# Kernel optimization log

Hardware: AMD Instinct MI355X
Metric: run time of the kernel (lower is better)

The kernel has to match this reference:

```python
import jax, jax.numpy as jnp
import numpy as np

N = 16384   # total nodes
E = 49152   # total edges (avg degree 3, molecular)
NG = 512    # graphs in batch
DIM = 64    # hidden dim
NF = 11     # node features
EF = 4      # edge features
HID = 128   # edge-MLP hidden
JUMPS = 3
S2S_STEPS = 3


def _gru_step(x, h, w_ih, w_hh, b_ih, b_hh):
    gi = x @ w_ih.T + b_ih
    gh = h @ w_hh.T + b_hh
    ir, iz, inn = jnp.split(gi, 3, axis=-1)
    hr, hz, hn = jnp.split(gh, 3, axis=-1)
    r = jax.nn.sigmoid(ir + hr)
    z = jax.nn.sigmoid(iz + hz)
    n = jnp.tanh(inn + r * hn)
    return (1.0 - z) * n + z * h


def _lstm_step(x, h, c, w_ih, w_hh, b_ih, b_hh):
    g = x @ w_ih.T + b_ih + h @ w_hh.T + b_hh
    i, f, gg, o = jnp.split(g, 4, axis=-1)
    c2 = jax.nn.sigmoid(f) * c + jax.nn.sigmoid(i) * jnp.tanh(gg)
    h2 = jax.nn.sigmoid(o) * jnp.tanh(c2)
    return h2, c2


def _segment_softmax(e, seg, num_segments):
    m = jax.ops.segment_max(e, seg, num_segments)
    ex = jnp.exp(e - m[seg])
    s = jax.ops.segment_sum(ex, seg, num_segments)
    return ex / s[seg]


def setup_inputs() -> dict:
    key = jax.random.key(0)
    ks = jax.random.split(key, 16)
    def rn(k, shape, s=0.05):
        return jax.random.normal(k, shape, jnp.float32) * s
    x = jax.random.normal(ks[0], (N, NF), jnp.float32)
    edge_attr = jax.random.uniform(ks[1], (E, EF), dtype=jnp.float32)
    edge_index = jax.random.randint(ks[2], (2, E), 0, N)
    batch = jnp.sort(jax.random.randint(ks[3], (N,), 0, NG))
    z = lambda n: jnp.zeros((n,), jnp.float32)
    return {
        "x": x, "edge_attr": edge_attr, "edge_index": edge_index, "batch": batch,
        "lin0_w": rn(ks[4], (DIM, NF)), "lin0_b": z(DIM),
        "mlp_w1": rn(ks[5], (HID, EF)), "mlp_b1": z(HID),
        "mlp_w2": rn(ks[6], (DIM * DIM, HID)), "mlp_b2": z(DIM * DIM),
        "conv_root": rn(ks[7], (DIM, DIM)), "conv_bias": z(DIM),
        "gru_w_ih": rn(ks[8], (3 * DIM, DIM)), "gru_w_hh": rn(ks[9], (3 * DIM, DIM)),
        "gru_b_ih": z(3 * DIM), "gru_b_hh": z(3 * DIM),
        "lstm_w_ih": rn(ks[10], (4 * DIM, 2 * DIM)), "lstm_w_hh": rn(ks[11], (4 * DIM, DIM)),
        "lstm_b_ih": z(4 * DIM), "lstm_b_hh": z(4 * DIM),
        "lin1_w": rn(ks[12], (DIM, 2 * DIM)), "lin1_b": z(DIM),
        "lin2_w": rn(ks[13], (1, DIM)), "lin2_b": z(1),
    }


def reference(x, edge_attr, edge_index, batch,
              lin0_w, lin0_b, mlp_w1, mlp_b1, mlp_w2, mlp_b2,
              conv_root, conv_bias,
              gru_w_ih, gru_w_hh, gru_b_ih, gru_b_hh,
              lstm_w_ih, lstm_w_hh, lstm_b_ih, lstm_b_hh,
              lin1_w, lin1_b, lin2_w, lin2_b):
    src, dst = edge_index[0], edge_index[1]
    out = jax.nn.relu(x @ lin0_w.T + lin0_b)           # [N, DIM]
    h = out
    # edge-conditioned weights: MLP(edge_attr) -> [E, DIM, DIM]
    ew = (jax.nn.relu(edge_attr @ mlp_w1.T + mlp_b1) @ mlp_w2.T + mlp_b2)
    ew = ew.reshape(E, DIM, DIM)
    deg = jnp.maximum(jax.ops.segment_sum(jnp.ones((E,), out.dtype), dst, N), 1.0)
    for _ in range(JUMPS):
        msg = jnp.einsum('ei,eio->eo', out[src], ew)    # gather + per-edge matvec
        agg = jax.ops.segment_sum(msg, dst, N) / deg[:, None]  # mean aggr
        m = jax.nn.relu(agg + out @ conv_root + conv_bias)
        h = _gru_step(m, h, gru_w_ih, gru_w_hh, gru_b_ih, gru_b_hh)
        out = h
    # Set2Set pooling
    qh = jnp.zeros((NG, DIM), out.dtype)
    qc = jnp.zeros((NG, DIM), out.dtype)
    q_star = jnp.zeros((NG, 2 * DIM), out.dtype)
    for _ in range(S2S_STEPS):
        qh, qc = _lstm_step(q_star, qh, qc, lstm_w_ih, lstm_w_hh, lstm_b_ih, lstm_b_hh)
        e = jnp.sum(out * qh[batch], axis=-1)           # [N]
        a = _segment_softmax(e, batch, NG)
        r = jax.ops.segment_sum(a[:, None] * out, batch, NG)  # [NG, DIM]
        q_star = jnp.concatenate([qh, r], axis=-1)
    o = jax.nn.relu(q_star @ lin1_w.T + lin1_b)
    return (o @ lin2_w.T + lin2_b).reshape(-1)
```

## Files before the change

### kernel.cpp

```cpp
#include <hip/hip_runtime.h>
#include <hip/hip_bf16.h>

#define NN 16384
#define NE 49152
#define NGR 512
#define DIM 64
#define NF 11
#define EF 4
#define HID 128
#define JUMPS 3
#define S2S 3
#define TE 192
#define SUP 49152

typedef _Float16 v8h __attribute__((ext_vector_type(8)));
typedef _Float16 v4h __attribute__((ext_vector_type(4)));
typedef float v4f __attribute__((ext_vector_type(4)));

__device__ __forceinline__ float sigmoidf_(float x) { return 1.0f / (1.0f + __expf(-x)); }

__device__ __forceinline__ void async16(const void* g, void* l) {
  __builtin_amdgcn_global_load_lds(
      (const __attribute__((address_space(1))) unsigned int*)g,
      (__attribute__((address_space(3))) unsigned int*)l, 16, 0, 0);
}

#define A0 (NN * DIM / 256)
#define A1 (A0 + NN / 256)
#define A2 (A1 + 112)
#define A3 (A2 + 192)
#define A4 (A3 + 32)
#define A5 (A4 + NN * DIM / 256)
#define A6 (A5 + 64 * 8192 / 256)
#define A7 (A6 + NE * HID / 256)
__global__ __launch_bounds__(256) void k_setup(const float* __restrict__ x,
                                               const float* __restrict__ l0w,
                                               const float* __restrict__ l0b,
                                               const float* __restrict__ ea,
                                               const float* __restrict__ w1,
                                               const float* __restrict__ b1,
                                               const float* __restrict__ w2,
                                               const float* __restrict__ conv_root,
                                               const float* __restrict__ gwih,
                                               const float* __restrict__ gwhh,
                                               const float* __restrict__ lwih,
                                               const float* __restrict__ lwhh,
                                               const float* __restrict__ l1w,
                                               float* __restrict__ out, float* __restrict__ h,
                                               _Float16* __restrict__ hid,
                                               _Float16* __restrict__ Tgo,
                                               _Float16* __restrict__ pCr,
                                               _Float16* __restrict__ pW,
                                               float* __restrict__ W2,
                                               float* __restrict__ l1T,
                                               float* __restrict__ agg, float* __restrict__ deg) {
  int b = blockIdx.x, tid = threadIdx.x;
  if (b < A0) { agg[b * 256 + tid] = 0.0f; return; }
  if (b < A1) { deg[(b - A0) * 256 + tid] = 0.0f; return; }
  if (b < A2) {
    int q = (b - A1) * 256 + tid;
    if (q < 4096) {
      int g = q >> 9, l = (q >> 3) & 63, j = q & 7;
      int ks = g >> 2, nt = g & 3;
      int k = ks * 32 + (l >> 4) * 8 + j, n = nt * 16 + (l & 15);
      pCr[q] = (_Float16)conv_root[k * 64 + n];
    } else if (q < 16384) {
      int q2 = q - 4096;
      int g = q2 >> 9, l = (q2 >> 3) & 63, j = q2 & 7;
      int ks = g / 12, nt = g % 12;
      int k = ks * 32 + (l >> 4) * 8 + j, n = nt * 16 + (l & 15);
      pW[q2] = (_Float16)gwih[n * 64 + k];
    } else {
      int q2 = q - 16384;
      int g = q2 >> 9, l = (q2 >> 3) & 63, j = q2 & 7;
      int ks = g / 12, nt = g % 12;
      int k = ks * 32 + (l >> 4) * 8 + j, n = nt * 16 + (l & 15);
      pW[12288 + q2] = (_Float16)gwhh[n * 64 + k];
    }
    return;
  }
  if (b < A3) {
    int i = (b - A2) * 256 + tid;
    int o = i / 192, k = i % 192;
    W2[i] = (k < 128) ? lwih[o * 128 + k] : lwhh[o * 64 + (k - 128)];
    return;
  }
  if (b < A4) { int i = (b - A3) * 256 + tid; int r = i / 128, c = i & 127; l1T[c * 64 + r] = l1w[i]; return; }
  if (b < A5) {
    int idx = (b - A4) * 256 + tid;
    int n = idx >> 6, d = idx & 63;
    float acc = l0b[d];
#pragma unroll
    for (int f = 0; f < NF; ++f) acc += x[n * NF + f] * l0w[d * NF + f];
    acc = fmaxf(acc, 0.0f);
    out[idx] = acc; h[idx] = acc;
    return;
  }
  if (b < A6) {
    int idx = (b - A5) * 256 + tid;
    float v = w2[idx];
    int row = idx >> 7, hh = idx & 127;
    int i = row >> 6, n = row & 63;
    int nt = n >> 4, col = n & 15;
    int ks = hh >> 5, quad = (hh >> 3) & 3, j = hh & 7;
    int t = i * 16 + ks * 4 + nt;
    Tgo[(size_t)t * 512 + (quad * 16 + col) * 8 + j] = (_Float16)v;
    return;
  }
  {
    int idx = (b - A6) * 256 + tid;
    int e = idx >> 7, hh = idx & 127;
    float acc = b1[hh];
#pragma unroll
    for (int f = 0; f < EF; ++f) acc += ea[e * EF + f] * w1[hh * EF + f];
    hid[idx] = (_Float16)fmaxf(acc, 0.0f);
  }
}

__global__ __launch_bounds__(768, 3) void k_conv(const float* __restrict__ out,
                                                 const _Float16* __restrict__ hid,
                                                 const _Float16* __restrict__ Tgo,
                                                 const int* __restrict__ src,
                                                 const int* __restrict__ dst,
                                                 float* __restrict__ agg,
                                                 float* __restrict__ deg, int count_deg) {
  __shared__ char sRing[2 * SUP];
  __shared__ _Float16 sT[64 * TE];
  __shared__ int sD[TE];
  int tid = threadIdx.x;
  int wv = tid >> 6, lane = tid & 63;
  int kh = wv & 1, nh = (wv >> 1) & 1, mh = wv >> 2;
  int col = lane & 15, quad = lane >> 4;
  int e0 = blockIdx.x * TE;
  int phase = blockIdx.x % 21;

  if (tid < TE) {
    int dn = dst[e0 + tid];
    sD[tid] = dn;
    if (count_deg) atomicAdd(&deg[dn], 1.0f);
  }
  {
    int row = tid >> 2, seg = tid & 3;
    int loc = row & 63;
    int base = (row & ~63) + (loc & 15) * 4 + (loc >> 4);
    const float* srow = out + (size_t)src[e0 + row] * DIM + seg * 16;
#pragma unroll
    for (int f = 0; f < 16; ++f)
      sT[(seg * 16 + f) * TE + base] = (_Float16)srow[f];
  }

  v8h hf[4][2];
#pragma unroll
  for (int ms = 0; ms < 4; ++ms) {
    const _Float16* hrow = hid + (size_t)(e0 + mh * 64 + ms * 16 + col) * HID + kh * 64 + quad * 8;
#pragma unroll
    for (int k2 = 0; k2 < 2; ++k2) hf[ms][k2] = *(const v8h*)(hrow + k2 * 32);
  }

  __syncthreads();
  asm volatile("s_waitcnt vmcnt(0)" ::: "memory");

  const char* TgoB = (const char*)Tgo;
#pragma unroll
  for (int p = 0; p < 2; ++p) {
    int op = phase + p; if (op >= 21) op -= 21;
    const char* gp = TgoB + (size_t)op * SUP + wv * 4096 + lane * 16;
    char* lp = sRing + p * SUP + wv * 4096;
#pragma unroll
    for (int j = 0; j < 4; ++j) async16(gp + j * 1024, lp + j * 1024);
  }

  v4f acc[4][2];
#pragma unroll
  for (int ms = 0; ms < 4; ++ms)
#pragma unroll
    for (int nt = 0; nt < 2; ++nt) acc[ms][nt] = (v4f)(0.0f);

  for (int t = 0; t < 21; ++t) {
    int ot = phase + t; if (ot >= 21) ot -= 21;
    if (t < 20) asm volatile("s_waitcnt vmcnt(4)" ::: "memory");
    else        asm volatile("s_waitcnt vmcnt(0)" ::: "memory");
    asm volatile("s_barrier" ::: "memory");
    const char* sbase = sRing + (t & 1) * SUP;
#pragma unroll
    for (int cc = 0; cc < 3; ++cc) {
      int sp = ot * 3 + cc;
      const char* rb = sbase + cc * 16384;
      v8h bfr[2][2];
#pragma unroll
      for (int k2 = 0; k2 < 2; ++k2)
#pragma unroll
        for (int nt = 0; nt < 2; ++nt)
          bfr[k2][nt] = *(const v8h*)(rb + (((kh * 2 + k2) * 4 + nh * 2 + nt) * 64 + lane) * 16);
      v4h s4 = *(const v4h*)&sT[sp * TE + mh * 64 + col * 4];
#pragma unroll
      for (int ms = 0; ms < 4; ++ms) {
        _Float16 sv = s4[ms];
        v8h s8 = {sv, sv, sv, sv, sv, sv, sv, sv};
#pragma unroll
        for (int k2 = 0; k2 < 2; ++k2) {
          v8h az = hf[ms][k2] * s8;
#pragma unroll
          for (int nt = 0; nt < 2; ++nt)
            acc[ms][nt] = __builtin_amdgcn_mfma_f32_16x16x32_f16(az, bfr[k2][nt], acc[ms][nt], 0, 0, 0);
        }
      }
    }
    asm volatile("s_waitcnt lgkmcnt(0)" ::: "memory");
    if (t + 2 < 21) {
      int o2 = phase + t + 2; if (o2 >= 21) o2 -= 21;
      const char* gp = TgoB + (size_t)o2 * SUP + wv * 4096 + lane * 16;
      char* lp = sRing + (t & 1) * SUP + wv * 4096;
#pragma unroll
      for (int j = 0; j < 4; ++j) async16(gp + j * 1024, lp + j * 1024);
    }
  }

  if (wv < 4) {
    const char* gp = TgoB + (size_t)63 * 16384 + wv * 4096 + lane * 16;
    char* lp = sRing + SUP + wv * 4096;
#pragma unroll
    for (int j = 0; j < 4; ++j) async16(gp + j * 1024, lp + j * 1024);
  }
  asm volatile("s_waitcnt vmcnt(0)" ::: "memory");
  asm volatile("s_barrier" ::: "memory");
  {
    const char* rb = sRing + SUP;
    v8h bfr[2][2];
#pragma unroll
    for (int k2 = 0; k2 < 2; ++k2)
#pragma unroll
      for (int nt = 0; nt < 2; ++nt)
        bfr[k2][nt] = *(const v8h*)(rb + (((kh * 2 + k2) * 4 + nh * 2 + nt) * 64 + lane) * 16);
    v4h s4 = *(const v4h*)&sT[63 * TE + mh * 64 + col * 4];
#pragma unroll
    for (int ms = 0; ms < 4; ++ms) {
      _Float16 sv = s4[ms];
      v8h s8 = {sv, sv, sv, sv, sv, sv, sv, sv};
#pragma unroll
      for (int k2 = 0; k2 < 2; ++k2) {
        v8h az = hf[ms][k2] * s8;
#pragma unroll
        for (int nt = 0; nt < 2; ++nt)
          acc[ms][nt] = __builtin_amdgcn_mfma_f32_16x16x32_f16(az, bfr[k2][nt], acc[ms][nt], 0, 0, 0);
      }
    }
  }

  __syncthreads();
  float* aggL = (float*)sRing;
  if (kh == 0) {
#pragma unroll
    for (int ms = 0; ms < 4; ++ms)
#pragma unroll
      for (int r = 0; r < 4; ++r) {
        int row = mh * 64 + ms * 16 + quad * 4 + r;
#pragma unroll
        for (int nt = 0; nt < 2; ++nt)
          aggL[row * 65 + (nh * 2 + nt) * 16 + col] = acc[ms][nt][r];
      }
  }
  __syncthreads();
  if (kh == 1) {
#pragma unroll
    for (int ms = 0; ms < 4; ++ms)
#pragma unroll
      for (int r = 0; r < 4; ++r) {
        int row = mh * 64 + ms * 16 + quad * 4 + r;
#pragma unroll
        for (int nt = 0; nt < 2; ++nt) {
          int a = row * 65 + (nh * 2 + nt) * 16 + col;
          aggL[a] += acc[ms][nt][r];
        }
      }
  }
  __syncthreads();
  for (int idx = tid; idx < TE * 64; idx += 768) {
    int row = idx >> 6, c = idx & 63;
    atomicAdd(agg + (size_t)sD[row] * DIM + c, aggL[row * 65 + c]);
  }
}

__global__ __launch_bounds__(256) void k_gru(float* __restrict__ agg,
                                             const float* __restrict__ deg,
                                             const _Float16* __restrict__ pCr,
                                             const _Float16* __restrict__ pW,
                                             const float* __restrict__ conv_bias,
                                             const float* __restrict__ bih,
                                             const float* __restrict__ bhh,
                                             float* __restrict__ out, float* __restrict__ h) {
  __shared__ _Float16 sW[24576];
  __shared__ _Float16 sMf[64][72];
  int tid = threadIdx.x;
  int w = tid >> 6, lane = tid & 63, col = lane & 15, quad = lane >> 4;
  int n0 = blockIdx.x * 64;
  int mrow = n0 + w * 16 + col;

  {
    int off = w * 12288 + lane * 16;
#pragma unroll
    for (int j = 0; j < 12; ++j)
      async16((const char*)pW + off + j * 1024, (char*)sW + off + j * 1024);
  }

  v8h afO[2], afH[2];
#pragma unroll
  for (int ks = 0; ks < 2; ++ks) {
    const float* p = out + (size_t)mrow * DIM + ks * 32 + quad * 8;
    float4 a = *(const float4*)p, b = *(const float4*)(p + 4);
    afO[ks] = (v8h){(_Float16)a.x, (_Float16)a.y, (_Float16)a.z, (_Float16)a.w,
                    (_Float16)b.x, (_Float16)b.y, (_Float16)b.z, (_Float16)b.w};
    const float* q = h + (size_t)mrow * DIM + ks * 32 + quad * 8;
    float4 c = *(const float4*)q, d = *(const float4*)(q + 4);
    afH[ks] = (v8h){(_Float16)c.x, (_Float16)c.y, (_Float16)c.z, (_Float16)c.w,
                    (_Float16)d.x, (_Float16)d.y, (_Float16)d.z, (_Float16)d.w};
  }

  v4f accC[4];
#pragma unroll
  for (int nt = 0; nt < 4; ++nt) accC[nt] = (v4f)(0.0f);
#pragma unroll
  for (int ks = 0; ks < 2; ++ks)
#pragma unroll
    for (int nt = 0; nt < 4; ++nt) {
      v8h bf = *(const v8h*)(pCr + (ks * 4 + nt) * 512 + lane * 8);
      accC[nt] = __builtin_amdgcn_mfma_f32_16x16x32_f16(afO[ks], bf, accC[nt], 0, 0, 0);
    }

#pragma unroll
  for (int r = 0; r < 4; ++r) {
    int nd = n0 + w * 16 + quad * 4 + r;
    float dg = fmaxf(deg[nd], 1.0f);
#pragma unroll
    for (int nt = 0; nt < 4; ++nt) {
      int o = nt * 16 + col;
      float mv = fmaxf(agg[(size_t)nd * DIM + o] / dg + accC[nt][r] + conv_bias[o], 0.0f);
      agg[(size_t)nd * DIM + o] = 0.0f;
      sMf[nd - n0][o] = (_Float16)mv;
    }
  }
  __syncthreads();

  v8h afM[2];
#pragma unroll
  for (int ks = 0; ks < 2; ++ks)
    afM[ks] = *(const v8h*)&sMf[w * 16 + col][ks * 32 + quad * 8];

  v4f aRZ[8], aIN[4], aHN[4];
#pragma unroll
  for (int t = 0; t < 8; ++t) aRZ[t] = (v4f)(0.0f);
#pragma unroll
  for (int t = 0; t < 4; ++t) { aIN[t] = (v4f)(0.0f); aHN[t] = (v4f)(0.0f); }
#pragma unroll
  for (int ks = 0; ks < 2; ++ks) {
#pragma unroll
    for (int nt = 0; nt < 8; ++nt) {
      v8h bf1 = *(const v8h*)(sW + (ks * 12 + nt) * 512 + lane * 8);
      aRZ[nt] = __builtin_amdgcn_mfma_f32_16x16x32_f16(afM[ks], bf1, aRZ[nt], 0, 0, 0);
      v8h bf2 = *(const v8h*)(sW + 12288 + (ks * 12 + nt) * 512 + lane * 8);
      aRZ[nt] = __builtin_amdgcn_mfma_f32_16x16x32_f16(afH[ks], bf2, aRZ[nt], 0, 0, 0);
    }
#pragma unroll
    for (int nt = 8; nt < 12; ++nt) {
      v8h bf1 = *(const v8h*)(sW + (ks * 12 + nt) * 512 + lane * 8);
      aIN[nt - 8] = __builtin_amdgcn_mfma_f32_16x16x32_f16(afM[ks], bf1, aIN[nt - 8], 0, 0, 0);
      v8h bf2 = *(const v8h*)(sW + 12288 + (ks * 12 + nt) * 512 + lane * 8);
      aHN[nt - 8] = __builtin_amdgcn_mfma_f32_16x16x32_f16(afH[ks], bf2, aHN[nt - 8], 0, 0, 0);
    }
  }

#pragma unroll
  for (int r = 0; r < 4; ++r) {
    int nd = n0 + w * 16 + quad * 4 + r;
#pragma unroll
    for (int nt = 0; nt < 4; ++nt) {
      int d = nt * 16 + col;
      float rv = sigmoidf_(aRZ[nt][r] + bih[d] + bhh[d]);
      float zv = sigmoidf_(aRZ[nt + 4][r] + bih[64 + d] + bhh[64 + d]);
      float nv = tanhf(aIN[nt][r] + bih[128 + d] + rv * (aHN[nt][r] + bhh[128 + d]));
      float hold = h[(size_t)nd * DIM + d];
      float hn = (1.0f - zv) * nv + zv * hold;
      h[(size_t)nd * DIM + d] = hn;
      out[(size_t)nd * DIM + d] = hn;
    }
  }
}

__global__ __launch_bounds__(256) void k_s2s(const float* __restrict__ out,
                                             const int* __restrict__ batch,
                                             const float* __restrict__ W2,
                                             const float* __restrict__ lbih,
                                             const float* __restrict__ lbhh,
                                             const float* __restrict__ l1T,
                                             const float* __restrict__ l1b,
                                             const float* __restrict__ l2w,
                                             const float* __restrict__ l2b,
                                             float* __restrict__ outp) {
  __shared__ float sOut[128][64];
  __shared__ __align__(16) float sQ[192];
  __shared__ float sQc[64], sG[256], sR[4][64], sEv[256];
  __shared__ float sMv, sSum;
  __shared__ int sRange[2];
  int g = blockIdx.x, tid = threadIdx.x;
  int wv = tid >> 6, ln = tid & 63;

  if (tid < 2) {
    int target = g + tid;
    int lo = 0, hi = NN;
    while (lo < hi) { int mid = (lo + hi) >> 1; if (batch[mid] < target) lo = mid + 1; else hi = mid; }
    sRange[tid] = lo;
  }
  if (tid < 192) sQ[tid] = 0.0f;
  if (tid < 64) sQc[tid] = 0.0f;
  __syncthreads();
  int s0 = sRange[0], cnt = sRange[1] - sRange[0];
  int stg = cnt < 128 ? cnt : 128;
  for (int r = wv; r < stg; r += 4) sOut[r][ln] = out[(size_t)(s0 + r) * DIM + ln];
  __syncthreads();

  const float* wrow = W2 + (size_t)tid * 192;
  float bias = lbih[tid] + lbhh[tid];

  for (int step = 0; step < S2S; ++step) {
    v4f a4[8];
#pragma unroll
    for (int s = 0; s < 8; ++s) a4[s] = (v4f)(0.0f);
#pragma unroll
    for (int kb = 0; kb < 48; ++kb) {
      v4f w4 = *(const v4f*)(wrow + kb * 4);
      v4f q4 = *(const v4f*)&sQ[kb * 4];
      a4[kb & 7] += w4 * q4;
    }
    v4f t4 = a4[0] + a4[1] + a4[2] + a4[3] + a4[4] + a4[5] + a4[6] + a4[7];
    sG[tid] = bias + t4[0] + t4[1] + t4[2] + t4[3];
    __syncthreads();
    if (tid < 64) {
      float gi = sG[tid], gf = sG[64 + tid], gg = sG[128 + tid], go = sG[192 + tid];
      float c2 = sigmoidf_(gf) * sQc[tid] + sigmoidf_(gi) * tanhf(gg);
      sQc[tid] = c2;
      sQ[128 + tid] = sigmoidf_(go) * tanhf(c2);
    }
    __syncthreads();
    for (int r = wv; r < cnt; r += 4) {
      float v = (r < 128) ? sOut[r][ln] : out[(size_t)(s0 + r) * DIM + ln];
      float p = v * sQ[128 + ln];
#pragma unroll
      for (int off = 32; off >= 1; off >>= 1) p += __shfl_xor(p, off);
      if (ln == 0 && r < 256) sEv[r] = p;
    }
    __syncthreads();
    if (wv == 0) {
      float mv = -1e30f;
      for (int r = ln; r < cnt; r += 64) mv = fmaxf(mv, sEv[r]);
#pragma unroll
      for (int off = 32; off >= 1; off >>= 1) mv = fmaxf(mv, __shfl_xor(mv, off));
      float ss = 0.0f;
      for (int r = ln; r < cnt; r += 64) ss += __expf(sEv[r] - mv);
#pragma unroll
      for (int off = 32; off >= 1; off >>= 1) ss += __shfl_xor(ss, off);
      if (ln == 0) { sMv = mv; sSum = ss; }
    }
    __syncthreads();
    float racc = 0.0f;
    for (int r = wv; r < cnt; r += 4) {
      float w = __expf(sEv[r] - sMv);
      float v = (r < 128) ? sOut[r][ln] : out[(size_t)(s0 + r) * DIM + ln];
      racc += w * v;
    }
    sR[wv][ln] = racc;
    __syncthreads();
    if (tid < 64) {
      float rv = sR[0][tid] + sR[1][tid] + sR[2][tid] + sR[3][tid];
      rv = (cnt > 0 && sSum > 0.0f) ? rv / sSum : 0.0f;
      sQ[tid] = sQ[128 + tid];
      sQ[64 + tid] = rv;
    }
    __syncthreads();
  }
  if (wv == 0) {
    float acc = l1b[ln];
#pragma unroll 4
    for (int k = 0; k < 128; ++k) acc += sQ[k] * l1T[k * 64 + ln];
    acc = fmaxf(acc, 0.0f);
    float p = acc * l2w[ln];
#pragma unroll
    for (int off = 32; off >= 1; off >>= 1) p += __shfl_xor(p, off);
    if (ln == 0) outp[g] = p + l2b[0];
  }
}

extern "C" void kernel_launch(void* const* d_in, const int* in_sizes, int n_in,
                              void* d_out, int out_size, void* d_ws, size_t ws_size,
                              hipStream_t stream) {
  const float* x         = (const float*)d_in[0];
  const float* ea        = (const float*)d_in[1];
  const int*   ei        = (const int*)d_in[2];
  const int*   batch     = (const int*)d_in[3];
  const float* lin0_w    = (const float*)d_in[4];
  const float* lin0_b    = (const float*)d_in[5];
  const float* w1        = (const float*)d_in[6];
  const float* b1        = (const float*)d_in[7];
  const float* w2        = (const float*)d_in[8];
  const float* conv_root = (const float*)d_in[10];
  const float* conv_bias = (const float*)d_in[11];
  const float* gwih      = (const float*)d_in[12];
  const float* gwhh      = (const float*)d_in[13];
  const float* gbih      = (const float*)d_in[14];
  const float* gbhh      = (const float*)d_in[15];
  const float* lwih      = (const float*)d_in[16];
  const float* lwhh      = (const float*)d_in[17];
  const float* lbih      = (const float*)d_in[18];
  const float* lbhh      = (const float*)d_in[19];
  const float* l1w       = (const float*)d_in[20];
  const float* l1b       = (const float*)d_in[21];
  const float* l2w       = (const float*)d_in[22];
  const float* l2b       = (const float*)d_in[23];
  float* outp = (float*)d_out;
  const int* srcI = ei;
  const int* dstI = ei + NE;

  char* ws = (char*)d_ws;
  size_t off = 0;
  auto alloc = [&](size_t bytes) -> char* {
    char* p = ws + off;
    off = (off + bytes + 255) & ~(size_t)255;
    return p;
  };
  _Float16* hid  = (_Float16*)alloc((size_t)NE * HID * 2);
  _Float16* Tgo  = (_Float16*)alloc((size_t)64 * 8192 * 2);
  float* out_  = (float*)alloc((size_t)NN * DIM * 4);
  float* h     = (float*)alloc((size_t)NN * DIM * 4);
  float* agg   = (float*)alloc((size_t)NN * DIM * 4);
  float* deg   = (float*)alloc((size_t)NN * 4);
  _Float16* pCr  = (_Float16*)alloc(8 * 512 * 2);
  _Float16* pW   = (_Float16*)alloc(48 * 512 * 2);
  float* W2m   = (float*)alloc(256 * 192 * 4);
  float* l1T   = (float*)alloc(64 * 128 * 4);
  (void)ws_size;

  dim3 B256(256), B768(768);

  k_setup<<<A7, B256, 0, stream>>>(x, lin0_w, lin0_b, ea, w1, b1, w2, conv_root,
                                   gwih, gwhh, lwih, lwhh, l1w, out_, h, hid, Tgo,
                                   pCr, pW, W2m, l1T, agg, deg);

  for (int jump = 0; jump < JUMPS; ++jump) {
    k_conv<<<NE / TE, B768, 0, stream>>>(out_, hid, Tgo, srcI, dstI, agg,
                                         deg, jump == 0 ? 1 : 0);
    k_gru<<<NN / 64, B256, 0, stream>>>(agg, deg, pCr, pW, conv_bias,
                                        gbih, gbhh, out_, h);
  }

  k_s2s<<<NGR, B256, 0, stream>>>(out_, batch, W2m, lbih, lbhh,
                                  l1T, l1b, l2w, l2b, outp);
}
```

Measured before the change: 338.8 us.

## Replace atomic scatter-add aggregation with per-node edge lists and gather in GRU

```diff
diff --git a/kernel.cpp b/kernel.cpp
--- a/kernel.cpp
+++ b/kernel.cpp
@@ -12,6 +12,7 @@
 #define S2S 3
 #define TE 192
 #define SUP 49152
+#define CAP 24
 
 typedef _Float16 v8h __attribute__((ext_vector_type(8)));
 typedef _Float16 v4h __attribute__((ext_vector_type(4)));
@@ -25,14 +26,12 @@
       (__attribute__((address_space(3))) unsigned int*)l, 16, 0, 0);
 }
 
-#define A0 (NN * DIM / 256)
-#define A1 (A0 + NN / 256)
-#define A2 (A1 + 112)
-#define A3 (A2 + 192)
-#define A4 (A3 + 32)
-#define A5 (A4 + NN * DIM / 256)
-#define A6 (A5 + 64 * 8192 / 256)
-#define A7 (A6 + NE * HID / 256)
+#define B0 (NN / 256)
+#define B1 (B0 + 112)
+#define B2 (B1 + 192)
+#define B3 (B2 + NN * DIM / 256)
+#define B4 (B3 + 64 * 8192 / 256)
+#define B5 (B4 + NE * HID / 256)
 __global__ __launch_bounds__(256) void k_setup(const float* __restrict__ x,
                                                const float* __restrict__ l0w,
                                                const float* __restrict__ l0b,
@@ -45,20 +44,17 @@
                                                const float* __restrict__ gwhh,
                                                const float* __restrict__ lwih,
                                                const float* __restrict__ lwhh,
-                                               const float* __restrict__ l1w,
                                                float* __restrict__ out, float* __restrict__ h,
                                                _Float16* __restrict__ hid,
                                                _Float16* __restrict__ Tgo,
                                                _Float16* __restrict__ pCr,
                                                _Float16* __restrict__ pW,
                                                float* __restrict__ W2,
-                                               float* __restrict__ l1T,
-                                               float* __restrict__ agg, float* __restrict__ deg) {
+                                               int* __restrict__ cnti) {
   int b = blockIdx.x, tid = threadIdx.x;
-  if (b < A0) { agg[b * 256 + tid] = 0.0f; return; }
-  if (b < A1) { deg[(b - A0) * 256 + tid] = 0.0f; return; }
-  if (b < A2) {
-    int q = (b - A1) * 256 + tid;
+  if (b < B0) { cnti[b * 256 + tid] = 0; return; }
+  if (b < B1) {
+    int q = (b - B0) * 256 + tid;
     if (q < 4096) {
       int g = q >> 9, l = (q >> 3) & 63, j = q & 7;
       int ks = g >> 2, nt = g & 3;
@@ -79,15 +75,14 @@
     }
     return;
   }
-  if (b < A3) {
-    int i = (b - A2) * 256 + tid;
+  if (b < B2) {
+    int i = (b - B1) * 256 + tid;
     int o = i / 192, k = i % 192;
     W2[i] = (k < 128) ? lwih[o * 128 + k] : lwhh[o * 64 + (k - 128)];
     return;
   }
-  if (b < A4) { int i = (b - A3) * 256 + tid; int r = i / 128, c = i & 127; l1T[c * 64 + r] = l1w[i]; return; }
-  if (b < A5) {
-    int idx = (b - A4) * 256 + tid;
+  if (b < B3) {
+    int idx = (b - B2) * 256 + tid;
     int n = idx >> 6, d = idx & 63;
     float acc = l0b[d];
 #pragma unroll
@@ -96,8 +91,8 @@
     out[idx] = acc; h[idx] = acc;
     return;
   }
-  if (b < A6) {
-    int idx = (b - A5) * 256 + tid;
+  if (b < B4) {
+    int idx = (b - B3) * 256 + tid;
     float v = w2[idx];
     int row = idx >> 7, hh = idx & 127;
     int i = row >> 6, n = row & 63;
@@ -108,25 +103,31 @@
     return;
   }
   {
-    int idx = (b - A6) * 256 + tid;
+    int idx = (b - B4) * 256 + tid;
     int e = idx >> 7, hh = idx & 127;
     float acc = b1[hh];
 #pragma unroll
     for (int f = 0; f < EF; ++f) acc += ea[e * EF + f] * w1[hh * EF + f];
     hid[idx] = (_Float16)fmaxf(acc, 0.0f);
   }
+}
+
+__global__ __launch_bounds__(256) void k_scatter(const int* __restrict__ dst,
+                                                 int* __restrict__ cnti,
+                                                 int* __restrict__ eidx) {
+  int e = blockIdx.x * 256 + threadIdx.x;
+  int d = dst[e];
+  int slot = atomicAdd(&cnti[d], 1);
+  if (slot < CAP) eidx[d * CAP + slot] = e;
 }
 
 __global__ __launch_bounds__(768, 3) void k_conv(const float* __restrict__ out,
                                                  const _Float16* __restrict__ hid,
                                                  const _Float16* __restrict__ Tgo,
                                                  const int* __restrict__ src,
-                                                 const int* __restrict__ dst,
-                                                 float* __restrict__ agg,
-                                                 float* __restrict__ deg, int count_deg) {
+                                                 float* __restrict__ msg) {
   __shared__ char sRing[2 * SUP];
   __shared__ _Float16 sT[64 * TE];
-  __shared__ int sD[TE];
   int tid = threadIdx.x;
   int wv = tid >> 6, lane = tid & 63;
   int kh = wv & 1, nh = (wv >> 1) & 1, mh = wv >> 2;
@@ -134,11 +135,6 @@
   int e0 = blockIdx.x * TE;
   int phase = blockIdx.x % 21;
 
-  if (tid < TE) {
-    int dn = dst[e0 + tid];
-    sD[tid] = dn;
-    if (count_deg) atomicAdd(&deg[dn], 1.0f);
-  }
   {
     int row = tid >> 2, seg = tid & 3;
     int loc = row & 63;
@@ -257,7 +253,7 @@
         int row = mh * 64 + ms * 16 + quad * 4 + r;
 #pragma unroll
         for (int nt = 0; nt < 2; ++nt)
-          aggL[row * 65 + (nh * 2 + nt) * 16 + col] = acc[ms][nt][r];
+          aggL[row * 66 + (nh * 2 + nt) * 16 + col] = acc[ms][nt][r];
       }
   }
   __syncthreads();
@@ -269,20 +265,22 @@
         int row = mh * 64 + ms * 16 + quad * 4 + r;
 #pragma unroll
         for (int nt = 0; nt < 2; ++nt) {
-          int a = row * 65 + (nh * 2 + nt) * 16 + col;
+          int a = row * 66 + (nh * 2 + nt) * 16 + col;
           aggL[a] += acc[ms][nt][r];
         }
       }
   }
   __syncthreads();
+  float* mrow = msg + (size_t)e0 * DIM;
   for (int idx = tid; idx < TE * 64; idx += 768) {
     int row = idx >> 6, c = idx & 63;
-    atomicAdd(agg + (size_t)sD[row] * DIM + c, aggL[row * 65 + c]);
-  }
-}
-
-__global__ __launch_bounds__(256) void k_gru(float* __restrict__ agg,
-                                             const float* __restrict__ deg,
+    mrow[idx] = aggL[row * 66 + c];
+  }
+}
+
+__global__ __launch_bounds__(256) void k_gru(const float* __restrict__ msg,
+                                             const int* __restrict__ eidx,
+                                             const int* __restrict__ cnti,
                                              const _Float16* __restrict__ pCr,
                                              const _Float16* __restrict__ pW,
                                              const float* __restrict__ conv_bias,
@@ -330,12 +328,20 @@
 #pragma unroll
   for (int r = 0; r < 4; ++r) {
     int nd = n0 + w * 16 + quad * 4 + r;
-    float dg = fmaxf(deg[nd], 1.0f);
+    int degN = cnti[nd];
+    float dg = fmaxf((float)degN, 1.0f);
+    int degC = degN < CAP ? degN : CAP;
+    float s0 = 0.f, s1 = 0.f, s2 = 0.f, s3 = 0.f;
+    const int* el = eidx + nd * CAP;
+    for (int j = 0; j < degC; ++j) {
+      const float* mr = msg + (size_t)el[j] * DIM + col;
+      s0 += mr[0]; s1 += mr[16]; s2 += mr[32]; s3 += mr[48];
+    }
+    float sv[4] = {s0, s1, s2, s3};
 #pragma unroll
     for (int nt = 0; nt < 4; ++nt) {
       int o = nt * 16 + col;
-      float mv = fmaxf(agg[(size_t)nd * DIM + o] / dg + accC[nt][r] + conv_bias[o], 0.0f);
-      agg[(size_t)nd * DIM + o] = 0.0f;
+      float mv = fmaxf(sv[nt] / dg + accC[nt][r] + conv_bias[o], 0.0f);
       sMf[nd - n0][o] = (_Float16)mv;
     }
   }
@@ -391,7 +397,7 @@
                                              const float* __restrict__ W2,
                                              const float* __restrict__ lbih,
                                              const float* __restrict__ lbhh,
-                                             const float* __restrict__ l1T,
+                                             const float* __restrict__ l1w,
                                              const float* __restrict__ l1b,
                                              const float* __restrict__ l2w,
                                              const float* __restrict__ l2b,
@@ -478,9 +484,18 @@
     __syncthreads();
   }
   if (wv == 0) {
-    float acc = l1b[ln];
-#pragma unroll 4
-    for (int k = 0; k < 128; ++k) acc += sQ[k] * l1T[k * 64 + ln];
+    const float* hrow = l1w + (size_t)ln * 128;
+    v4f h4[4];
+#pragma unroll
+    for (int s = 0; s < 4; ++s) h4[s] = (v4f)(0.0f);
+#pragma unroll
+    for (int kb = 0; kb < 32; ++kb) {
+      v4f w4 = *(const v4f*)(hrow + kb * 4);
+      v4f q4 = *(const v4f*)&sQ[kb * 4];
+      h4[kb & 3] += w4 * q4;
+    }
+    v4f u4 = h4[0] + h4[1] + h4[2] + h4[3];
+    float acc = l1b[ln] + u4[0] + u4[1] + u4[2] + u4[3];
     acc = fmaxf(acc, 0.0f);
     float p = acc * l2w[ln];
 #pragma unroll
@@ -530,27 +545,27 @@
   _Float16* Tgo  = (_Float16*)alloc((size_t)64 * 8192 * 2);
   float* out_  = (float*)alloc((size_t)NN * DIM * 4);
   float* h     = (float*)alloc((size_t)NN * DIM * 4);
-  float* agg   = (float*)alloc((size_t)NN * DIM * 4);
-  float* deg   = (float*)alloc((size_t)NN * 4);
+  float* msg   = (float*)alloc((size_t)NE * DIM * 4);
+  int*   eidx  = (int*)alloc((size_t)NN * CAP * 4);
+  int*   cnti  = (int*)alloc((size_t)NN * 4);
   _Float16* pCr  = (_Float16*)alloc(8 * 512 * 2);
   _Float16* pW   = (_Float16*)alloc(48 * 512 * 2);
   float* W2m   = (float*)alloc(256 * 192 * 4);
-  float* l1T   = (float*)alloc(64 * 128 * 4);
   (void)ws_size;
 
   dim3 B256(256), B768(768);
 
-  k_setup<<<A7, B256, 0, stream>>>(x, lin0_w, lin0_b, ea, w1, b1, w2, conv_root,
-                                   gwih, gwhh, lwih, lwhh, l1w, out_, h, hid, Tgo,
-                                   pCr, pW, W2m, l1T, agg, deg);
+  k_setup<<<B5, B256, 0, stream>>>(x, lin0_w, lin0_b, ea, w1, b1, w2, conv_root,
+                                   gwih, gwhh, lwih, lwhh, out_, h, hid, Tgo,
+                                   pCr, pW, W2m, cnti);
+  k_scatter<<<NE / 256, B256, 0, stream>>>(dstI, cnti, eidx);
 
   for (int jump = 0; jump < JUMPS; ++jump) {
-    k_conv<<<NE / TE, B768, 0, stream>>>(out_, hid, Tgo, srcI, dstI, agg,
-                                         deg, jump == 0 ? 1 : 0);
-    k_gru<<<NN / 64, B256, 0, stream>>>(agg, deg, pCr, pW, conv_bias,
+    k_conv<<<NE / TE, B768, 0, stream>>>(out_, hid, Tgo, srcI, msg);
+    k_gru<<<NN / 64, B256, 0, stream>>>(msg, eidx, cnti, pCr, pW, conv_bias,
                                         gbih, gbhh, out_, h);
   }
 
   k_s2s<<<NGR, B256, 0, stream>>>(out_, batch, W2m, lbih, lbhh,
-                                  l1T, l1b, l2w, l2b, outp);
-}
+                                  l1w, l1b, l2w, l2b, outp);
+}
```

After: 363.5 us. 1.07x slower.
